# Kernel tuning notes

Hardware: AMD Instinct MI355X
Metric: run time of the kernel (lower is better)

The kernel has to match this reference:

```python
import jax, jax.numpy as jnp
import numpy as np
from jax.scipy.special import gammaln, logsumexp

T, K, D = 262144, 32, 64


def setup_inputs() -> dict:
    key = jax.random.key(0)
    ks = jax.random.split(key, 7)
    Y = jax.random.normal(ks[0], (T, D), dtype=jnp.float32)
    dT = jax.random.uniform(ks[1], (T,), dtype=jnp.float32) + 0.01  # strictly positive intervals
    A = jax.random.normal(ks[2], (K, K), dtype=jnp.float32)
    log_ab = jax.random.normal(ks[3], (K, 2), dtype=jnp.float32) * 0.5
    mu = jax.random.normal(ks[4], (K, D), dtype=jnp.float32)
    log_sigma = jax.random.normal(ks[5], (K, D), dtype=jnp.float32) * 0.1
    pi = jax.random.normal(ks[6], (K,), dtype=jnp.float32)
    return {"Y": Y, "dT": dT, "A": A, "log_ab": log_ab, "mu": mu, "log_sigma": log_sigma, "pi": pi}


def _gamma_ll(dT, log_ab):
    # per-state Gamma(concentration=exp(log_ab[:,0]), rate=exp(log_ab[:,1])) log_prob -> [T, K]
    a = jnp.exp(log_ab[:, 0])
    b = jnp.exp(log_ab[:, 1])
    const = a * log_ab[:, 1] - gammaln(a)  # a*log(b) - lgamma(a)
    return const[None, :] + jnp.log(dT)[:, None] * (a - 1.0)[None, :] - dT[:, None] * b[None, :]


def _gauss_ll(Y, mu, log_sigma):
    # diagonal-Gaussian emission log-likelihood summed over D, via GEMMs -> [T, K]
    inv_var = jnp.exp(-2.0 * log_sigma)  # [K, D]
    quad = (-0.5) * (Y * Y) @ inv_var.T + Y @ (mu * inv_var).T - 0.5 * jnp.sum(mu * mu * inv_var, axis=-1)[None, :]
    const = -jnp.sum(log_sigma, axis=-1) - 0.5 * D * jnp.log(2.0 * jnp.pi).astype(Y.dtype)
    return quad + const[None, :]


def _hmm_lognorm(pi0, logA, ll):
    # log-domain forward algorithm; returns log normalizer (scalar)
    alpha0 = pi0 + ll[0]

    def step(alpha, ll_t):
        # alpha_t[j] = logsumexp_i(alpha[i] + logA[i, j]) + ll_t[j]
        alpha = logsumexp(alpha[:, None] + logA, axis=0) + ll_t
        return alpha, None

    alphaT, _ = jax.lax.scan(step, alpha0, ll[1:])
    return logsumexp(alphaT)


def reference(Y, dT, A, log_ab, mu, log_sigma, pi):
    h = Y  # obs_model embedding (identity for Gaussian emission model)
    y_ll = _gauss_ll(Y, mu, log_sigma)          # [T, K]
    y_loss = jnp.zeros((), dtype=Y.dtype)
    dT_ll = _gamma_ll(dT, log_ab)               # [T, K]
    ll = y_ll + dT_ll
    logA = jax.nn.log_softmax(A, axis=1)        # LogSoftmax(dim=1)(A)
    pi0 = jax.nn.log_softmax(pi, axis=0)        # LogSoftmax(dim=0)(pi)
    loss = -1.0 * _hmm_lognorm(pi0, logA, ll) + y_loss
    return h, loss
```

## Files before the change

### kernel.cpp

```cpp
#include <hip/hip_runtime.h>
#include <stdint.h>

#define TT 262144
#define KK 32
#define DD 64
#define LSTEP 32
#define PCH 8192
#define YSTRIDE 68

typedef __attribute__((ext_vector_type(4)))  float f4v;
typedef __attribute__((ext_vector_type(16))) float f16v;
typedef __attribute__((ext_vector_type(4)))  short s4v;
typedef __attribute__((ext_vector_type(8)))  short s8v;
typedef __attribute__((ext_vector_type(8)))  __bf16 bf8v;
typedef __attribute__((ext_vector_type(2)))  unsigned int u2v;
typedef __attribute__((ext_vector_type(4)))  unsigned int u4v;

#define WS_AFRAG_US 0
#define WS_WFRAG_US 1024
#define WS_WF    2560
#define WS_CK    6656
#define WS_AM1   6688
#define WS_BB    6720
#define WS_PI0   6752
#define WS_LS    8192
#define WS_LS2   16384
#define SH_MATS  33280
#define SH_MATS2 (33280 + PCH*1024)
#define LN2F 0.69314718055994531f

__device__ __forceinline__ unsigned pkbf(float hi, float lo) {
    return __builtin_amdgcn_perm(__builtin_bit_cast(unsigned, hi),
                                 __builtin_bit_cast(unsigned, lo), 0x07060302u);
}
__device__ __forceinline__ unsigned short f2bf_rne(float f) {
    unsigned u = __builtin_bit_cast(unsigned, f);
    unsigned r = u + 0x7FFFu + ((u >> 16) & 1u);
    return (unsigned short)(r >> 16);
}
__device__ __forceinline__ float bf2f(unsigned short u) {
    return __builtin_bit_cast(float, (unsigned)u << 16);
}
__device__ __forceinline__ float wmax32(float v) {
    v = fmaxf(v, __shfl_xor(v, 1));  v = fmaxf(v, __shfl_xor(v, 2));
    v = fmaxf(v, __shfl_xor(v, 4));  v = fmaxf(v, __shfl_xor(v, 8));
    v = fmaxf(v, __shfl_xor(v, 16));
    return v;
}
__device__ __forceinline__ float wmax64(float v) {
    v = wmax32(v); v = fmaxf(v, __shfl_xor(v, 32));
    return v;
}
__device__ __forceinline__ float wsum32(float v) {
    v += __shfl_xor(v, 1); v += __shfl_xor(v, 2); v += __shfl_xor(v, 4);
    v += __shfl_xor(v, 8); v += __shfl_xor(v, 16);
    return v;
}
__device__ __forceinline__ float wsum64(float v) {
    v = wsum32(v); v += __shfl_xor(v, 32);
    return v;
}
__device__ __forceinline__ float wval(int dd, int k, const float* mu, const float* lsg) {
    int d = dd & 63;
    float lv = lsg[k * DD + d];
    float iv = __expf(-2.f * lv);
    return (dd < DD) ? (-0.5f * iv) : (mu[k * DD + d] * iv);
}
__device__ __forceinline__ f16v mfma16(s8v a, s8v b, f16v c) {
    return __builtin_amdgcn_mfma_f32_32x32x16_bf16(
        __builtin_bit_cast(bf8v, a), __builtin_bit_cast(bf8v, b), c, 0, 0, 0);
}

__global__ void k0_prep(const float* __restrict__ Y, const float* __restrict__ A,
                        const float* __restrict__ lab, const float* __restrict__ mu,
                        const float* __restrict__ lsg, const float* __restrict__ pi,
                        float* __restrict__ ws, float* __restrict__ out)
{
    __shared__ float lseA[KK];
    const int tid = threadIdx.x;
    if (tid < KK) {
        float m = -1e30f;
        for (int j = 0; j < KK; ++j) m = fmaxf(m, A[tid * KK + j]);
        float s = 0.f;
        for (int j = 0; j < KK; ++j) s += __expf(A[tid * KK + j] - m);
        lseA[tid] = m + __logf(s);

        float mp = -1e30f;
        for (int j = 0; j < KK; ++j) mp = fmaxf(mp, pi[j]);
        float sp = 0.f;
        for (int j = 0; j < KK; ++j) sp += __expf(pi[j] - mp);
        ws[WS_PI0 + tid] = pi[tid] - (mp + __logf(sp));

        float la = lab[tid * 2 + 0], lb = lab[tid * 2 + 1];
        float a = __expf(la), b = __expf(lb);
        float c1 = 0.f, c2 = 0.f;
        for (int d = 0; d < DD; ++d) {
            float lv = lsg[tid * DD + d];
            float mv = mu[tid * DD + d];
            c1 -= lv;
            c2 += mv * mv * __expf(-2.f * lv);
        }
        ws[WS_CK + tid]  = a * lb - lgammaf(a) + c1 - 0.5f * c2 - 32.f * 1.8378770664093453f;
        ws[WS_AM1 + tid] = a - 1.f;
        ws[WS_BB + tid]  = b;
    }
    __syncthreads();
    unsigned short* us = (unsigned short*)ws;
    for (int idx = tid; idx < 1024; idx += 256) {
        int g2 = idx >> 9, rem = idx & 511, ln = rem >> 3, e = rem & 7;
        int m = 16 * g2 + 8 * (e >> 2) + 4 * (ln >> 5) + (e & 3), i = ln & 31;
        us[WS_AFRAG_US + idx] = f2bf_rne(__expf(A[m * KK + i] - lseA[m]));
    }
    for (int idx = tid; idx < 4096; idx += 256) {
        int s2 = idx >> 9, rem = idx & 511, ln = rem >> 3, e = rem & 7;
        int dd = 16 * s2 + 8 * (e >> 2) + 4 * (ln >> 5) + (e & 3);
        us[WS_WFRAG_US + idx] = f2bf_rne(wval(dd, ln & 31, mu, lsg));
    }
    for (int idx = tid; idx < 4096; idx += 256) {
        int dd = idx >> 5, k = idx & 31;
        ws[WS_WF + idx] = wval(dd, k, mu, lsg);
    }
    if (tid < DD) out[tid] = Y[tid];
}

__global__ __launch_bounds__(256, 4) void k1_scan(
    const float* __restrict__ Y, const float* __restrict__ dTp,
    float* __restrict__ ws, float* __restrict__ out)
{
    __shared__ __align__(16) float Yt[4][32 * YSTRIDE];
    __shared__ __align__(16) float dtv[4][32], dtl[4][32];

    const int tid = threadIdx.x;
    const int wv = tid >> 6, l = tid & 63, h = l >> 5, c = l & 31;
    const int p = blockIdx.x * 4 + wv;
    const int t0 = 1 + p * LSTEP;
    const int nsteps = min(LSTEP, TT - t0);

    const unsigned short* afr = (const unsigned short*)ws + WS_AFRAG_US;
    const unsigned short* wfr = (const unsigned short*)ws + WS_WFRAG_US;

    const float cK = ws[WS_CK + c], am1 = ws[WS_AM1 + c], bb = ws[WS_BB + c];

    if (l < 32) {
        int t = t0 + l;
        float dv = (t < TT) ? dTp[t] : 1.f;
        dtv[wv][l] = dv;
        dtl[wv][l] = __logf(dv);
    }

    f16v zf;
    #pragma unroll
    for (int r = 0; r < 16; ++r) zf[r] = 0.f;

    {
        const size_t gbase = (size_t)t0 * DD;
        const int r = (l >> 4);
        const int col = (l & 15) * 4;
        #pragma unroll
        for (int i = 0; i < 8; ++i) {
            const size_t gi = gbase + (size_t)i * 256 + l * 4;
            f4v y4; y4[0] = 0.f; y4[1] = 0.f; y4[2] = 0.f; y4[3] = 0.f;
            const bool ok = gi < (size_t)TT * DD;
            if (ok) y4 = *(const f4v*)(Y + gi);
            if (ok) *(f4v*)(out + gi) = y4;
            *(f4v*)(&Yt[wv][(i * 4 + r) * YSTRIDE + col]) = y4;
        }
    }

    f16v acc = zf;
    s8v raws[4];
    #pragma unroll
    for (int g2 = 0; g2 < 4; ++g2) {
        const f4v y0 = *(const f4v*)(&Yt[wv][c * YSTRIDE + 16 * g2 + 4 * h]);
        const f4v y1 = *(const f4v*)(&Yt[wv][c * YSTRIDE + 16 * g2 + 8 + 4 * h]);
        const f4v q0 = y0 * y0, q1 = y1 * y1;
        u4v sqp, rwp;
        sqp[0] = pkbf(q0[1], q0[0]); sqp[1] = pkbf(q0[3], q0[2]);
        sqp[2] = pkbf(q1[1], q1[0]); sqp[3] = pkbf(q1[3], q1[2]);
        rwp[0] = pkbf(y0[1], y0[0]); rwp[1] = pkbf(y0[3], y0[2]);
        rwp[2] = pkbf(y1[1], y1[0]); rwp[3] = pkbf(y1[3], y1[2]);
        raws[g2] = __builtin_bit_cast(s8v, rwp);
        s8v wf = *(const s8v*)(wfr + g2 * 512 + l * 8);
        acc = mfma16(__builtin_bit_cast(s8v, sqp), wf, acc);
    }
    #pragma unroll
    for (int g2 = 0; g2 < 4; ++g2) {
        s8v wf = *(const s8v*)(wfr + (4 + g2) * 512 + l * 8);
        acc = mfma16(raws[g2], wf, acc);
    }

    const s8v aF0 = *(const s8v*)(afr + l * 8);
    const s8v aF1 = *(const s8v*)(afr + 512 + l * 8);

    float csv = 0.f;
    #pragma unroll
    for (int m = 0; m < 4; ++m) {
        const f4v dv4 = *(const f4v*)(&dtv[wv][8 * m + 4 * h]);
        const f4v dl4 = *(const f4v*)(&dtl[wv][8 * m + 4 * h]);
        #pragma unroll
        for (int j = 0; j < 4; ++j) {
            const int row = 8 * m + 4 * h + j;
            float llv = acc[4 * m + j] + cK + am1 * dl4[j] - bb * dv4[j];
            float cm = wmax32(llv);
            Yt[wv][row * YSTRIDE + c] = __expf(llv - cm);
            csv += (row < nsteps) ? cm : 0.f;
        }
    }
    float cacc = wsum64(csv) * (1.f / 32.f);

    asm volatile("s_waitcnt lgkmcnt(0)" ::: "memory");

    f16v S;
    #pragma unroll
    for (int m = 0; m < 4; ++m)
        #pragma unroll
        for (int j = 0; j < 4; ++j)
            S[4 * m + j] = ((8 * m + 4 * h + j) == c) ? 1.f : 0.f;
    float l2acc = 0.f;

    auto step = [&](int n) {
        u4v b0, b1;
        b0[0] = pkbf(S[1],  S[0]);  b0[1] = pkbf(S[3],  S[2]);
        b0[2] = pkbf(S[5],  S[4]);  b0[3] = pkbf(S[7],  S[6]);
        b1[0] = pkbf(S[9],  S[8]);  b1[1] = pkbf(S[11], S[10]);
        b1[2] = pkbf(S[13], S[12]); b1[3] = pkbf(S[15], S[14]);
        f16v Dv = mfma16(aF0, __builtin_bit_cast(s8v, b0), zf);
        Dv = mfma16(aF1, __builtin_bit_cast(s8v, b1), Dv);
        #pragma unroll
        for (int m = 0; m < 4; ++m) {
            const f4v e4 = *(const f4v*)(&Yt[wv][n * YSTRIDE + 8 * m + 4 * h]);
            S[4 * m + 0] = Dv[4 * m + 0] * e4[0];
            S[4 * m + 1] = Dv[4 * m + 1] * e4[1];
            S[4 * m + 2] = Dv[4 * m + 2] * e4[2];
            S[4 * m + 3] = Dv[4 * m + 3] * e4[3];
        }
    };
    auto rescale = [&]() {
        float mx = S[0];
        #pragma unroll
        for (int r = 1; r < 16; ++r) mx = fmaxf(mx, S[r]);
        mx = wmax64(mx);
        const float inv = __fdividef(1.f, mx);
        #pragma unroll
        for (int r = 0; r < 16; ++r) S[r] *= inv;
        l2acc += __log2f(mx);
    };

    if (p != PCH - 1) {
        #pragma unroll
        for (int n = 0; n < LSTEP; ++n) {
            step(n);
            if ((n & 3) == 3) rescale();
        }
    } else {
        for (int n = 0; n < nsteps; ++n) {
            step(n);
            if ((n & 3) == 3) rescale();
        }
    }

    unsigned short* Tb = (unsigned short*)&Yt[wv][0];
    asm volatile("s_waitcnt lgkmcnt(0)" ::: "memory");
    #pragma unroll
    for (int m = 0; m < 4; ++m)
        #pragma unroll
        for (int j = 0; j < 4; ++j)
            Tb[(8 * m + 4 * h + j) * 36 + c] = f2bf_rne(S[4 * m + j]);
    asm volatile("s_waitcnt lgkmcnt(0)" ::: "memory");
    u2v tg0 = *(const u2v*)(Tb + c * 36 + 0  + 4 * h);
    u2v tg1 = *(const u2v*)(Tb + c * 36 + 8  + 4 * h);
    u2v tg2 = *(const u2v*)(Tb + c * 36 + 16 + 4 * h);
    u2v tg3 = *(const u2v*)(Tb + c * 36 + 24 + 4 * h);
    unsigned short* gm = (unsigned short*)ws + SH_MATS + (size_t)p * 1024 + l * 16;
    u4v s0; s0[0] = tg0[0]; s0[1] = tg0[1]; s0[2] = tg1[0]; s0[3] = tg1[1];
    u4v s1; s1[0] = tg2[0]; s1[1] = tg2[1]; s1[2] = tg3[0]; s1[3] = tg3[1];
    *(u4v*)(gm) = s0;
    *(u4v*)(gm + 8) = s1;
    if (l == 0) ws[WS_LS + p] = cacc + LN2F * l2acc;
}

__device__ __forceinline__ f16v prodAU(const u4v a0, const u4v a1, const f16v U, const f16v zf) {
    u4v b0, b1;
    b0[0] = pkbf(U[1],  U[0]);  b0[1] = pkbf(U[3],  U[2]);
    b0[2] = pkbf(U[5],  U[4]);  b0[3] = pkbf(U[7],  U[6]);
    b1[0] = pkbf(U[9],  U[8]);  b1[1] = pkbf(U[11], U[10]);
    b1[2] = pkbf(U[13], U[12]); b1[3] = pkbf(U[15], U[14]);
    f16v Dv = mfma16(__builtin_bit_cast(s8v, a0), __builtin_bit_cast(s8v, b0), zf);
    Dv = mfma16(__builtin_bit_cast(s8v, a1), __builtin_bit_cast(s8v, b1), Dv);
    return Dv;
}

__global__ __launch_bounds__(128, 1) void k2_combine(float* __restrict__ ws)
{
    __shared__ __align__(16) unsigned short slot[2][1152];
    __shared__ float scl[2], lac[2];
    const int tid = threadIdx.x, wv = tid >> 6, l = tid & 63, h = l >> 5, c = l & 31;
    const int blk = blockIdx.x;
    const int idx0 = blk * 64 + wv * 32;
    const unsigned short* mats = (const unsigned short*)ws + SH_MATS;

    float lsv = (l < 32) ? ws[WS_LS + idx0 + l] : 0.f;
    float lssum = wsum64(lsv);

    f16v zf;
    #pragma unroll
    for (int r = 0; r < 16; ++r) zf[r] = 0.f;
    f16v U;
    #pragma unroll
    for (int m = 0; m < 4; ++m)
        #pragma unroll
        for (int j = 0; j < 4; ++j)
            U[4 * m + j] = ((8 * m + 4 * h + j) == c) ? 1.f : 0.f;
    float l2a = 0.f;

    u4v pf[2][2];
    {
        const u4v* mp0 = (const u4v*)(mats + (size_t)idx0 * 1024) + l * 2;
        const u4v* mp1 = (const u4v*)(mats + (size_t)(idx0 + 1) * 1024) + l * 2;
        pf[0][0] = mp0[0]; pf[0][1] = mp0[1];
        pf[1][0] = mp1[0]; pf[1][1] = mp1[1];
    }
    for (int q = 0; q < 32; ++q) {
        const u4v a0 = pf[q & 1][0], a1 = pf[q & 1][1];
        if (q + 2 < 32) {
            const u4v* mp = (const u4v*)(mats + (size_t)(idx0 + q + 2) * 1024) + l * 2;
            pf[q & 1][0] = mp[0]; pf[q & 1][1] = mp[1];
        }
        f16v Dv = prodAU(a0, a1, U, zf);
        if ((q & 3) == 3) {
            float mx = Dv[0];
            #pragma unroll
            for (int r = 1; r < 16; ++r) mx = fmaxf(mx, Dv[r]);
            mx = wmax64(mx);
            const float inv = __fdividef(1.f, mx);
            #pragma unroll
            for (int r = 0; r < 16; ++r) U[r] = Dv[r] * inv;
            l2a += __log2f(mx);
        } else {
            U = Dv;
        }
    }
    #pragma unroll
    for (int m = 0; m < 4; ++m)
        #pragma unroll
        for (int j = 0; j < 4; ++j)
            slot[wv][(8 * m + 4 * h + j) * 36 + c] = f2bf_rne(U[4 * m + j]);
    if (l == 0) { scl[wv] = lssum; lac[wv] = l2a; }
    __syncthreads();

    if (wv == 0) {
        u4v a0, a1;
        {
            u2v t0 = *(const u2v*)(&slot[1][c * 36 + 0 + 4 * h]);
            u2v t1 = *(const u2v*)(&slot[1][c * 36 + 8 + 4 * h]);
            u2v t2 = *(const u2v*)(&slot[1][c * 36 + 16 + 4 * h]);
            u2v t3 = *(const u2v*)(&slot[1][c * 36 + 24 + 4 * h]);
            a0[0] = t0[0]; a0[1] = t0[1]; a0[2] = t1[0]; a0[3] = t1[1];
            a1[0] = t2[0]; a1[1] = t2[1]; a1[2] = t3[0]; a1[3] = t3[1];
        }
        f16v Dv = prodAU(a0, a1, U, zf);
        float mx = Dv[0];
        #pragma unroll
        for (int r = 1; r < 16; ++r) mx = fmaxf(mx, Dv[r]);
        mx = wmax64(mx);
        const float inv = __fdividef(1.f, mx);
        #pragma unroll
        for (int r = 0; r < 16; ++r) U[r] = Dv[r] * inv;
        const float l2tot = lac[0] + lac[1] + __log2f(mx);
        asm volatile("s_waitcnt lgkmcnt(0)" ::: "memory");
        #pragma unroll
        for (int m = 0; m < 4; ++m)
            #pragma unroll
            for (int j = 0; j < 4; ++j)
                slot[0][(8 * m + 4 * h + j) * 36 + c] = f2bf_rne(U[4 * m + j]);
        asm volatile("s_waitcnt lgkmcnt(0)" ::: "memory");
        u2v tg[4];
        #pragma unroll
        for (int g = 0; g < 4; ++g)
            tg[g] = *(const u2v*)(&slot[0][c * 36 + 8 * g + 4 * h]);
        unsigned short* gm = (unsigned short*)ws + SH_MATS2 + (size_t)blk * 1024 + l * 16;
        u4v s0; s0[0] = tg[0][0]; s0[1] = tg[0][1]; s0[2] = tg[1][0]; s0[3] = tg[1][1];
        u4v s1; s1[0] = tg[2][0]; s1[1] = tg[2][1]; s1[2] = tg[3][0]; s1[3] = tg[3][1];
        *(u4v*)(gm) = s0;
        *(u4v*)(gm + 8) = s1;
        if (l == 0) ws[WS_LS2 + blk] = scl[0] + scl[1] + LN2F * l2tot;
    }
}

__global__ __launch_bounds__(1024, 1) void k3_final(
    const float* __restrict__ Y, const float* __restrict__ dTp,
    float* __restrict__ ws, float* __restrict__ out)
{
    __shared__ __align__(16) unsigned short slot[16][1152];
    __shared__ float sc[16];
    const int tid = threadIdx.x, wv = tid >> 6, l = tid & 63, h = l >> 5, c = l & 31;
    const unsigned short* mats2 = (const unsigned short*)ws + SH_MATS2;

    f16v zf;
    #pragma unroll
    for (int r = 0; r < 16; ++r) zf[r] = 0.f;

    const int idx0 = wv * 8;
    float lsv = (l < 8) ? ws[WS_LS2 + idx0 + l] : 0.f;
    float lssum = wsum64(lsv);
    f16v U;
    #pragma unroll
    for (int m = 0; m < 4; ++m)
        #pragma unroll
        for (int j = 0; j < 4; ++j)
            U[4 * m + j] = ((8 * m + 4 * h + j) == c) ? 1.f : 0.f;
    float l2a = 0.f;
    u4v pf[2][2];
    {
        const u4v* mp0 = (const u4v*)(mats2 + (size_t)idx0 * 1024) + l * 2;
        const u4v* mp1 = (const u4v*)(mats2 + (size_t)(idx0 + 1) * 1024) + l * 2;
        pf[0][0] = mp0[0]; pf[0][1] = mp0[1];
        pf[1][0] = mp1[0]; pf[1][1] = mp1[1];
    }
    for (int q = 0; q < 8; ++q) {
        const u4v a0 = pf[q & 1][0], a1 = pf[q & 1][1];
        if (q + 2 < 8) {
            const u4v* mp = (const u4v*)(mats2 + (size_t)(idx0 + q + 2) * 1024) + l * 2;
            pf[q & 1][0] = mp[0]; pf[q & 1][1] = mp[1];
        }
        f16v Dv = prodAU(a0, a1, U, zf);
        if ((q & 3) == 3) {
            float mx = Dv[0];
            #pragma unroll
            for (int r = 1; r < 16; ++r) mx = fmaxf(mx, Dv[r]);
            mx = wmax64(mx);
            const float inv = __fdividef(1.f, mx);
            #pragma unroll
            for (int r = 0; r < 16; ++r) U[r] = Dv[r] * inv;
            l2a += __log2f(mx);
        } else {
            U = Dv;
        }
    }
    #pragma unroll
    for (int m = 0; m < 4; ++m)
        #pragma unroll
        for (int j = 0; j < 4; ++j)
            slot[wv][(8 * m + 4 * h + j) * 36 + c] = f2bf_rne(U[4 * m + j]);
    if (l == 0) sc[wv] = lssum + LN2F * l2a;
    __syncthreads();

    for (int s = 1; s < 16; s <<= 1) {
        const int cnt = 16 / (2 * s);
        if (wv < cnt) {
            const int i = wv * 2 * s;
            s8v aA0, aA1, bB0, bB1;
            {
                u2v t0 = *(const u2v*)(&slot[i + s][c * 36 + 0 + 4 * h]);
                u2v t1 = *(const u2v*)(&slot[i + s][c * 36 + 8 + 4 * h]);
                u2v t2 = *(const u2v*)(&slot[i + s][c * 36 + 16 + 4 * h]);
                u2v t3 = *(const u2v*)(&slot[i + s][c * 36 + 24 + 4 * h]);
                u4v a0; a0[0] = t0[0]; a0[1] = t0[1]; a0[2] = t1[0]; a0[3] = t1[1];
                u4v a1; a1[0] = t2[0]; a1[1] = t2[1]; a1[2] = t3[0]; a1[3] = t3[1];
                aA0 = __builtin_bit_cast(s8v, a0);
                aA1 = __builtin_bit_cast(s8v, a1);
                #pragma unroll
                for (int j = 0; j < 4; ++j) {
                    bB0[j]     = (short)slot[i][(0  + 4 * h + j) * 36 + c];
                    bB0[4 + j] = (short)slot[i][(8  + 4 * h + j) * 36 + c];
                    bB1[j]     = (short)slot[i][(16 + 4 * h + j) * 36 + c];
                    bB1[4 + j] = (short)slot[i][(24 + 4 * h + j) * 36 + c];
                }
            }
            f16v Dv = mfma16(aA0, bB0, zf);
            Dv = mfma16(aA1, bB1, Dv);
            float mx = Dv[0];
            #pragma unroll
            for (int r = 1; r < 16; ++r) mx = fmaxf(mx, Dv[r]);
            mx = wmax64(mx);
            const float inv = __fdividef(1.f, mx);
            #pragma unroll
            for (int m = 0; m < 4; ++m)
                #pragma unroll
                for (int j = 0; j < 4; ++j)
                    slot[i][(8 * m + 4 * h + j) * 36 + c] = f2bf_rne(Dv[4 * m + j] * inv);
            if (l == 0) sc[i] = sc[i] + sc[i + s] + __logf(mx);
        }
        __syncthreads();
    }

    if (wv == 0) {
        float acc = 0.f;
        const float* Wf = ws + WS_WF;
        for (int dd = 0; dd < 128; ++dd) {
            const float yv = Y[dd & 63];
            const float f = (dd < 64) ? yv * yv : yv;
            acc = fmaf(f, Wf[dd * 32 + c], acc);
        }
        const float dt0 = dTp[0];
        const float ll0 = acc + ws[WS_CK + c] + ws[WS_AM1 + c] * __logf(dt0) - ws[WS_BB + c] * dt0;
        const float av = ws[WS_PI0 + c] + ll0;
        const float c0 = wmax32(av);
        const float a0 = __expf(av - c0);
        float part = 0.f;
        #pragma unroll
        for (int i = 0; i < 16; ++i) {
            const int ii = 16 * h + i;
            const float m = bf2f(slot[0][c * 36 + ii]);
            const float ai = __shfl(a0, ii);
            part = fmaf(m, ai, part);
        }
        const float srow = part + __shfl_xor(part, 32);
        const float tot = wsum32(srow);
        if (l == 0) out[(size_t)TT * DD] = -(sc[0] + c0 + __logf(tot));
    }
}

extern "C" void kernel_launch(void* const* d_in, const int* in_sizes, int n_in,
                              void* d_out, int out_size, void* d_ws, size_t ws_size,
                              hipStream_t stream)
{
    const float* Y   = (const float*)d_in[0];
    const float* dTp = (const float*)d_in[1];
    const float* A   = (const float*)d_in[2];
    const float* lab = (const float*)d_in[3];
    const float* mu  = (const float*)d_in[4];
    const float* lsg = (const float*)d_in[5];
    const float* pi  = (const float*)d_in[6];
    float* out = (float*)d_out;
    float* ws  = (float*)d_ws;

    hipLaunchKernelGGL(k0_prep, dim3(1), dim3(256), 0, stream, Y, A, lab, mu, lsg, pi, ws, out);
    hipLaunchKernelGGL(k1_scan, dim3(PCH / 4), dim3(256), 0, stream, Y, dTp, ws, out);
    hipLaunchKernelGGL(k2_combine, dim3(128), dim3(128), 0, stream, ws);
    hipLaunchKernelGGL(k3_final, dim3(1), dim3(1024), 0, stream, Y, dTp, ws, out);
}
```

Before: 188.4 us.

## Stage Y tile as bf16 MFMA fragments in LDS to raise occupancy

The scan kernel now converts each loaded Y chunk to bf16 and writes it straight into LDS in MFMA-fragment order, instead of keeping a padded fp32 tile and repacking it later. This shrinks per-wave LDS from 32x68 floats to 1152 floats, and launch bounds go from 4 to 6 blocks per CU to exploit the freed space. The squared term is now computed from the bf16-rounded Y, which adds a little extra rounding error. The higher occupancy target may also cap registers and cause spills.

Result: no change. 188.6 us (+0.1%).

```diff
diff --git a/kernel.cpp b/kernel.cpp
--- a/kernel.cpp
+++ b/kernel.cpp
@@ -6,7 +6,6 @@
 #define DD 64
 #define LSTEP 32
 #define PCH 8192
-#define YSTRIDE 68
 
 typedef __attribute__((ext_vector_type(4)))  float f4v;
 typedef __attribute__((ext_vector_type(16))) float f16v;
@@ -123,11 +122,11 @@
     if (tid < DD) out[tid] = Y[tid];
 }
 
-__global__ __launch_bounds__(256, 4) void k1_scan(
+__global__ __launch_bounds__(256, 6) void k1_scan(
     const float* __restrict__ Y, const float* __restrict__ dTp,
     float* __restrict__ ws, float* __restrict__ out)
 {
-    __shared__ __align__(16) float Yt[4][32 * YSTRIDE];
+    __shared__ __align__(16) float Ebuf[4][1152];
     __shared__ __align__(16) float dtv[4][32], dtl[4][32];
 
     const int tid = threadIdx.x;
@@ -152,40 +151,47 @@
     #pragma unroll
     for (int r = 0; r < 16; ++r) zf[r] = 0.f;
 
+    unsigned short* Ybf = (unsigned short*)&Ebuf[wv][0];
+    float* E = &Ebuf[wv][0];
+
     {
         const size_t gbase = (size_t)t0 * DD;
-        const int r = (l >> 4);
-        const int col = (l & 15) * 4;
+        const int rr = l & 3, cb = l >> 2;
+        const int g2s = cb >> 2, bs = (cb >> 1) & 1, hs = cb & 1;
         #pragma unroll
         for (int i = 0; i < 8; ++i) {
-            const size_t gi = gbase + (size_t)i * 256 + l * 4;
+            const size_t gi = gbase + (size_t)i * 256 + (size_t)(rr * 64 + cb * 4);
             f4v y4; y4[0] = 0.f; y4[1] = 0.f; y4[2] = 0.f; y4[3] = 0.f;
             const bool ok = gi < (size_t)TT * DD;
             if (ok) y4 = *(const f4v*)(Y + gi);
             if (ok) *(f4v*)(out + gi) = y4;
-            *(f4v*)(&Yt[wv][(i * 4 + r) * YSTRIDE + col]) = y4;
-        }
-    }
+            const int row = i * 4 + rr;
+            const int off = g2s * 512 + (32 * hs + row) * 8 + 4 * bs;
+            u2v pw; pw[0] = pkbf(y4[1], y4[0]); pw[1] = pkbf(y4[3], y4[2]);
+            *(u2v*)(Ybf + off) = pw;
+        }
+    }
+    asm volatile("s_waitcnt lgkmcnt(0)" ::: "memory");
 
     f16v acc = zf;
     s8v raws[4];
     #pragma unroll
     for (int g2 = 0; g2 < 4; ++g2) {
-        const f4v y0 = *(const f4v*)(&Yt[wv][c * YSTRIDE + 16 * g2 + 4 * h]);
-        const f4v y1 = *(const f4v*)(&Yt[wv][c * YSTRIDE + 16 * g2 + 8 + 4 * h]);
-        const f4v q0 = y0 * y0, q1 = y1 * y1;
-        u4v sqp, rwp;
-        sqp[0] = pkbf(q0[1], q0[0]); sqp[1] = pkbf(q0[3], q0[2]);
-        sqp[2] = pkbf(q1[1], q1[0]); sqp[3] = pkbf(q1[3], q1[2]);
-        rwp[0] = pkbf(y0[1], y0[0]); rwp[1] = pkbf(y0[3], y0[2]);
-        rwp[2] = pkbf(y1[1], y1[0]); rwp[3] = pkbf(y1[3], y1[2]);
-        raws[g2] = __builtin_bit_cast(s8v, rwp);
-        s8v wf = *(const s8v*)(wfr + g2 * 512 + l * 8);
-        acc = mfma16(__builtin_bit_cast(s8v, sqp), wf, acc);
+        const s8v yf = *(const s8v*)(Ybf + g2 * 512 + l * 8);
+        raws[g2] = yf;
+        u4v qp;
+        #pragma unroll
+        for (int e2 = 0; e2 < 4; ++e2) {
+            const float f0 = bf2f((unsigned short)yf[2 * e2]);
+            const float f1 = bf2f((unsigned short)yf[2 * e2 + 1]);
+            qp[e2] = pkbf(f1 * f1, f0 * f0);
+        }
+        const s8v wf = *(const s8v*)(wfr + g2 * 512 + l * 8);
+        acc = mfma16(__builtin_bit_cast(s8v, qp), wf, acc);
     }
     #pragma unroll
     for (int g2 = 0; g2 < 4; ++g2) {
-        s8v wf = *(const s8v*)(wfr + (4 + g2) * 512 + l * 8);
+        const s8v wf = *(const s8v*)(wfr + (4 + g2) * 512 + l * 8);
         acc = mfma16(raws[g2], wf, acc);
     }
 
@@ -202,7 +208,7 @@
             const int row = 8 * m + 4 * h + j;
             float llv = acc[4 * m + j] + cK + am1 * dl4[j] - bb * dv4[j];
             float cm = wmax32(llv);
-            Yt[wv][row * YSTRIDE + c] = __expf(llv - cm);
+            E[row * 36 + c] = __expf(llv - cm);
             csv += (row < nsteps) ? cm : 0.f;
         }
     }
@@ -228,7 +234,7 @@
         Dv = mfma16(aF1, __builtin_bit_cast(s8v, b1), Dv);
         #pragma unroll
         for (int m = 0; m < 4; ++m) {
-            const f4v e4 = *(const f4v*)(&Yt[wv][n * YSTRIDE + 8 * m + 4 * h]);
+            const f4v e4 = *(const f4v*)(E + n * 36 + 8 * m + 4 * h);
             S[4 * m + 0] = Dv[4 * m + 0] * e4[0];
             S[4 * m + 1] = Dv[4 * m + 1] * e4[1];
             S[4 * m + 2] = Dv[4 * m + 2] * e4[2];
@@ -259,7 +265,7 @@
         }
     }
 
-    unsigned short* Tb = (unsigned short*)&Yt[wv][0];
+    unsigned short* Tb = (unsigned short*)&Ebuf[wv][0];
     asm volatile("s_waitcnt lgkmcnt(0)" ::: "memory");
     #pragma unroll
     for (int m = 0; m < 4; ++m)
```
